# Performance work log

Hardware: AMD Instinct MI355X
Metric: run time of the kernel (lower is better)

## Reference

```python
import jax, jax.numpy as jnp
import numpy as np

B, N, K, E = 4096, 64, 128, 512  # batch, n_cont_cols, max_num_buckets, embed_dim
EPS = 1e-8


def setup_inputs() -> dict:
    key = jax.random.key(0)
    kx, kw = jax.random.split(key)
    X = jax.random.uniform(kx, (B, N), dtype=jnp.float32)  # values in [0,1)
    # 129 sorted boundaries per column spanning [0,1] (same for every column)
    boundaries = jnp.tile(jnp.linspace(0.0, 1.0, K + 1, dtype=jnp.float32)[None, :], (N, 1))
    weight = jax.random.normal(kw, (N, K, E), dtype=jnp.float32) * 0.01  # init.normal_(std=0.01)
    bias = jnp.zeros((N, E), dtype=jnp.float32)  # init.zeros_
    return {"X": X, "boundaries": boundaries, "weight": weight, "bias": bias}


def reference(X, boundaries, weight, bias):
    # X: [B,N], boundaries: [N,K+1] sorted, weight: [N,K,E], bias: [N,E]
    Bn, Nc = X.shape
    Kb = weight.shape[1]
    # torch.bucketize(feat, bnd[1:-1], right=False) == searchsorted(side='left'); result in [0, K-1]
    inner = boundaries[:, 1:-1]  # [N, K-1]
    bidx = jax.vmap(lambda b, f: jnp.searchsorted(b, f, side='left'),
                    in_axes=(0, 1), out_axes=1)(inner, X)  # [B,N] int32
    cols = jnp.arange(Nc)[None, :]  # [1,N]
    start = boundaries[cols, bidx]        # [B,N]
    end = boundaries[cols, bidx + 1]      # [B,N]
    frac = (X - start) / (end - start + EPS)  # fractional position within bucket
    # greater_mask[b,n,k] = float(X[b,n] > boundaries[n,k]) for k in [0, K-1]
    greater = (X[:, :, None] > boundaries[None, :, :-1]).astype(X.dtype)  # [B,N,K]
    # scatter-assign frac at each sample's bucket index
    mask = jnp.where(jnp.arange(Kb)[None, None, :] == bidx[:, :, None],
                     frac[:, :, None], greater)  # [B,N,K]
    x = jnp.einsum('bnk,nke->bne', mask, weight) + bias[None]  # [B,N,E]
    x = jax.nn.relu(x)  # activation_fn='relu'
    # nn.Dropout is identity in eval mode
    return x
```

## Files before the change

### kernel.cpp

```cpp
#include <hip/hip_runtime.h>


#define BB 4096
#define NN 64
#define KK 128
#define EE 512
#define EPSF 1e-8f

__global__ void cumsum_kernel(const float* __restrict__ weight,
                              const float* __restrict__ bias,
                              float* __restrict__ C) {
    int n = blockIdx.x >> 1;
    int e = ((blockIdx.x & 1) << 8) + threadIdx.x;
    const float* w = weight + ((size_t)n * KK) * EE + e;
    float*       c = C + ((size_t)n * (KK + 1)) * EE + e;
    float run = bias[n * EE + e];
    c[0] = run;
#pragma unroll 8
    for (int k = 0; k < KK; ++k) {
        run += w[(size_t)k * EE];
        c[(size_t)(k + 1) * EE] = run;
    }
}

__global__ void idx_kernel(const float* __restrict__ X,
                           const float* __restrict__ boundaries,
                           int* __restrict__ bidx_out,
                           float* __restrict__ frac_out) {
    int i = blockIdx.x * blockDim.x + threadIdx.x;
    int n = i & (NN - 1);
    float x = X[i];
    const float* bnd = boundaries + n * (KK + 1);
    int lo = 0, hi = KK - 1;
    while (lo < hi) {
        int mid = (lo + hi) >> 1;
        if (bnd[1 + mid] < x) lo = mid + 1; else hi = mid;
    }
    float start = bnd[lo];
    float end   = bnd[lo + 1];
    bidx_out[i] = lo;
    frac_out[i] = (x - start) / (end - start + EPSF);
}

__global__ void gather_kernel(const float* __restrict__ C,
                              const int* __restrict__ bidx,
                              const float* __restrict__ frac,
                              float* __restrict__ out) {
    int base = blockIdx.x << 2;
    int e = threadIdx.x << 1;
#pragma unroll
    for (int it = 0; it < 4; ++it) {
        int t = base + it;
        int n = t >> 12;
        int b = t & (BB - 1);
        int i = b * NN + n;
        int bi = __ldg(&bidx[i]);
        float f = __ldg(&frac[i]);
        const float2* c0 =
            (const float2*)(C + (((size_t)n * (KK + 1) + bi) * EE) + e);
        float2 lo = c0[0];
        float2 hi = c0[EE / 2];
        float2 r;
        r.x = fmaf(f, hi.x - lo.x, lo.x);
        r.y = fmaf(f, hi.y - lo.y, lo.y);
        r.x = fmaxf(r.x, 0.f);
        r.y = fmaxf(r.y, 0.f);
        *(float2*)(out + ((size_t)b * NN + n) * EE + e) = r;
    }
}

extern "C" void kernel_launch(void* const* d_in, const int* in_sizes, int n_in,
                              void* d_out, int out_size, void* d_ws, size_t ws_size,
                              hipStream_t stream) {
    const float* X          = (const float*)d_in[0];
    const float* boundaries = (const float*)d_in[1];
    const float* weight     = (const float*)d_in[2];
    const float* bias       = (const float*)d_in[3];
    float* out = (float*)d_out;

    float* C = (float*)d_ws;
    size_t Csz = (size_t)NN * (KK + 1) * EE;
    int*   bidx = (int*)(C + Csz);
    float* frac = (float*)(bidx + (size_t)BB * NN);

    cumsum_kernel<<<NN * (EE / 256), 256, 0, stream>>>(weight, bias, C);
    idx_kernel<<<(BB * NN) / 256, 256, 0, stream>>>(X, boundaries, bidx, frac);
    gather_kernel<<<(BB * NN) / 4, 256, 0, stream>>>(C, bidx, frac, out);
}
```

Baseline: 595.5 us.

## Restructure gather to per-batch rows with float4 nontemporal stores and precomputed offsets

```diff
diff --git a/kernel.cpp b/kernel.cpp
--- a/kernel.cpp
+++ b/kernel.cpp
@@ -7,25 +7,27 @@
 #define EE 512
 #define EPSF 1e-8f
 
+typedef float f32x4 __attribute__((ext_vector_type(4)));
+
 __global__ void cumsum_kernel(const float* __restrict__ weight,
                               const float* __restrict__ bias,
                               float* __restrict__ C) {
-    int n = blockIdx.x >> 1;
-    int e = ((blockIdx.x & 1) << 8) + threadIdx.x;
+    int n = blockIdx.x >> 2;
+    int e = ((blockIdx.x & 3) << 7) + threadIdx.x;
     const float* w = weight + ((size_t)n * KK) * EE + e;
     float*       c = C + ((size_t)n * (KK + 1)) * EE + e;
     float run = bias[n * EE + e];
     c[0] = run;
 #pragma unroll 8
     for (int k = 0; k < KK; ++k) {
-        run += w[(size_t)k * EE];
+        run += __builtin_nontemporal_load(w + (size_t)k * EE);
         c[(size_t)(k + 1) * EE] = run;
     }
 }
 
 __global__ void idx_kernel(const float* __restrict__ X,
                            const float* __restrict__ boundaries,
-                           int* __restrict__ bidx_out,
+                           int* __restrict__ off_out,
                            float* __restrict__ frac_out) {
     int i = blockIdx.x * blockDim.x + threadIdx.x;
     int n = i & (NN - 1);
@@ -38,34 +40,32 @@
     }
     float start = bnd[lo];
     float end   = bnd[lo + 1];
-    bidx_out[i] = lo;
+    off_out[i]  = (n * (KK + 1) + lo) * EE;
     frac_out[i] = (x - start) / (end - start + EPSF);
 }
 
 __global__ void gather_kernel(const float* __restrict__ C,
-                              const int* __restrict__ bidx,
+                              const int* __restrict__ off_arr,
                               const float* __restrict__ frac,
                               float* __restrict__ out) {
-    int base = blockIdx.x << 2;
-    int e = threadIdx.x << 1;
-#pragma unroll
-    for (int it = 0; it < 4; ++it) {
-        int t = base + it;
-        int n = t >> 12;
-        int b = t & (BB - 1);
+    int half = threadIdx.x >> 7;
+    int ev   = threadIdx.x & 127;
+    int b    = (blockIdx.x << 1) + half;
+#pragma unroll 4
+    for (int n = 0; n < NN; ++n) {
         int i = b * NN + n;
-        int bi = __ldg(&bidx[i]);
-        float f = __ldg(&frac[i]);
-        const float2* c0 =
-            (const float2*)(C + (((size_t)n * (KK + 1) + bi) * EE) + e);
-        float2 lo = c0[0];
-        float2 hi = c0[EE / 2];
-        float2 r;
-        r.x = fmaf(f, hi.x - lo.x, lo.x);
-        r.y = fmaf(f, hi.y - lo.y, lo.y);
-        r.x = fmaxf(r.x, 0.f);
-        r.y = fmaxf(r.y, 0.f);
-        *(float2*)(out + ((size_t)b * NN + n) * EE + e) = r;
+        int off = off_arr[i];
+        float f = frac[i];
+        const f32x4* p = (const f32x4*)(C + off) + ev;
+        f32x4 lo = p[0];
+        f32x4 hi = p[EE / 4];
+        f32x4 r;
+        r.x = fmaxf(fmaf(f, hi.x - lo.x, lo.x), 0.f);
+        r.y = fmaxf(fmaf(f, hi.y - lo.y, lo.y), 0.f);
+        r.z = fmaxf(fmaf(f, hi.z - lo.z, lo.z), 0.f);
+        r.w = fmaxf(fmaf(f, hi.w - lo.w, lo.w), 0.f);
+        f32x4* o = (f32x4*)(out + ((size_t)b * NN + n) * EE) + ev;
+        __builtin_nontemporal_store(r, o);
     }
 }
 
@@ -80,10 +80,10 @@
 
     float* C = (float*)d_ws;
     size_t Csz = (size_t)NN * (KK + 1) * EE;
-    int*   bidx = (int*)(C + Csz);
-    float* frac = (float*)(bidx + (size_t)BB * NN);
+    int*   off  = (int*)(C + Csz);
+    float* frac = (float*)(off + (size_t)BB * NN);
 
-    cumsum_kernel<<<NN * (EE / 256), 256, 0, stream>>>(weight, bias, C);
-    idx_kernel<<<(BB * NN) / 256, 256, 0, stream>>>(X, boundaries, bidx, frac);
-    gather_kernel<<<(BB * NN) / 4, 256, 0, stream>>>(C, bidx, frac, out);
+    cumsum_kernel<<<NN * (EE / 128), 128, 0, stream>>>(weight, bias, C);
+    idx_kernel<<<(BB * NN) / 256, 256, 0, stream>>>(X, boundaries, off, frac);
+    gather_kernel<<<BB / 2, 256, 0, stream>>>(C, off, frac, out);
 }
```

Measured after the change: 619.3 us. 4.0% more time.
